# Kernel tuning notes

Hardware: AMD Instinct MI355X
Metric: run time of the kernel (lower is better)

Reference implementation:

```python
import jax, jax.numpy as jnp
import numpy as np

VOCAB_SIZE = 8192
EMBED_DIM = 256


def setup_inputs() -> dict:
    key = jax.random.key(0)
    k1, k2 = jax.random.split(key)
    N = 16384  # batch(512) * num_slots(8) * tokens_per_slot(4)
    z = jax.random.normal(k1, (N, EMBED_DIM), dtype=jnp.float32)
    codebook = jax.random.normal(k2, (VOCAB_SIZE, EMBED_DIM), dtype=jnp.float32)
    return {"z": z, "codebook": codebook}


def reference(z, codebook):
    # Squared-distance cdist via the expansion ||z||^2 + ||e||^2 - 2 z.e^T
    z_sq = jnp.sum(z * z, axis=1, keepdims=True)            # [N, 1]
    e_sq = jnp.sum(codebook * codebook, axis=1)              # [V]
    dist = z_sq + e_sq - 2.0 * jnp.matmul(z, codebook.T)     # [N, V]
    tokens = jnp.argmin(dist, axis=-1)                       # [N] int
    z_q = codebook[tokens]                                   # [N, E] gather
    # one-hot reference count (side statistic in the original forward)
    ref_count = jnp.zeros((VOCAB_SIZE,), dtype=jnp.float32).at[tokens].add(1.0)
    return tokens, z_q, ref_count
```

## Files before the change

kernel.cpp:

```cpp
#include <hip/hip_runtime.h>
#include <math.h>

#define N_ROWS 16384
#define VOCAB  8192
#define EMB    256

#define BM 128
#define BV 128
#define BK 64
#define VSPLIT 8
#define VRANGE (VOCAB / VSPLIT)
#define NVT    (VRANGE / BV)
#define TAU 0.15f

typedef _Float16 half8 __attribute__((ext_vector_type(8)));
typedef _Float16 half4 __attribute__((ext_vector_type(4)));
typedef float floatx4 __attribute__((ext_vector_type(4)));

__device__ __forceinline__ void load_lds16(const _Float16* g, _Float16* l) {
    __builtin_amdgcn_global_load_lds(
        (const __attribute__((address_space(1))) void*)g,
        (__attribute__((address_space(3))) void*)l, 16, 0, 0);
}

__global__ void prep_kernel(const float* __restrict__ z, const float* __restrict__ cb,
                            _Float16* __restrict__ zh, _Float16* __restrict__ ch,
                            float* __restrict__ esq, float* __restrict__ cnt,
                            unsigned long long* __restrict__ rkey,
                            int* __restrict__ flagcnt) {
    const int b = blockIdx.x, t = threadIdx.x;
    if (b < VOCAB / 4) {
        const int row  = b * 4 + (t >> 6);
        const int lane = t & 63;
        const float4 f = *(const float4*)(cb + (size_t)row * EMB + lane * 4);
        half4 h;
        h.x = (_Float16)f.x; h.y = (_Float16)f.y; h.z = (_Float16)f.z; h.w = (_Float16)f.w;
        *(half4*)(ch + (size_t)row * EMB + lane * 4) = h;
        float s = f.x * f.x + f.y * f.y + f.z * f.z + f.w * f.w;
        #pragma unroll
        for (int off = 32; off > 0; off >>= 1) s += __shfl_down(s, off, 64);
        if (lane == 0) esq[row] = s;
        if (t < 4) cnt[b * 4 + t] = 0.0f;
        if (t >= 8 && t < 16) rkey[b * 8 + (t - 8)] = ~0ull;
        if (b == 0 && t == 4) flagcnt[0] = 0;
        if (b == 0 && t == 5) flagcnt[1] = 0;
    } else {
        const size_t idx4 = (size_t)(b - VOCAB / 4) * 256 + t;
        const float4 f = *(const float4*)(z + idx4 * 4);
        half4 h;
        h.x = (_Float16)f.x; h.y = (_Float16)f.y; h.z = (_Float16)f.z; h.w = (_Float16)f.w;
        *(half4*)(zh + idx4 * 4) = h;
    }
}

__global__ __launch_bounds__(256, 2)
void mfma_dist_kernel(const _Float16* __restrict__ zh, const _Float16* __restrict__ ch,
                      const float* __restrict__ esq,
                      float* __restrict__ pd1, float* __restrict__ pd2,
                      float* __restrict__ pd3,
                      int* __restrict__ pi1, int* __restrict__ pi2) {
    __shared__ _Float16 zs[BM * BK];
    __shared__ _Float16 cs[BV * BK];
    float* sc_d1 = (float*)zs;
    float* sc_d2 = sc_d1 + BM * 2;
    float* sc_d3 = sc_d2 + BM * 2;
    int*   sc_i1 = (int*)(sc_d3 + BM * 2);
    int*   sc_i2 = sc_i1 + BM * 2;

    const int row0  = blockIdx.x * BM;
    const int vbase = blockIdx.y * VRANGE;

    const int tid  = threadIdx.x;
    const int w    = tid >> 6;
    const int lane = tid & 63;
    const int lr   = lane & 15;
    const int quad = lane >> 4;
    const int mh   = (w >> 1) * 64;
    const int vh   = (w & 1) * 64;

    const int q7   = quad ^ (lr & 7);
    const int offA0 = q7 * 8;
    const int offA1 = (4 ^ q7) * 8;
    int rA[4], rB[4];
    #pragma unroll
    for (int i = 0; i < 4; ++i) { rA[i] = (mh + i * 16 + lr) * BK; rB[i] = (vh + i * 16 + lr) * BK; }

    const int schunk = (lane & 7) ^ (lane >> 3);
    const _Float16* zsrc = zh + (size_t)(row0 + w * 32 + (lane >> 3)) * EMB + schunk * 8;

    float m1[16], m2[16], m3[16];
    #pragma unroll
    for (int t = 0; t < 16; ++t) { m1[t] = -INFINITY; m2[t] = -INFINITY; m3[t] = -INFINITY; }

    float ev[4];
    #pragma unroll
    for (int j = 0; j < 4; ++j) ev[j] = esq[vbase + vh + j * 16 + lr];

    for (int vt = 0; vt < NVT; ++vt) {
        const int v0 = vbase + vt * BV;
        const _Float16* csrc = ch + (size_t)(v0 + w * 32 + (lane >> 3)) * EMB + schunk * 8;

        floatx4 acc[4][4];
        #pragma unroll
        for (int j = 0; j < 4; ++j) {
            const float e2 = -0.5f * ev[j];
            #pragma unroll
            for (int i = 0; i < 4; ++i) acc[i][j] = (floatx4)e2;
        }
        float evn[4];
        {
            const int vtn = (vt + 1 < NVT) ? vt + 1 : vt;
            #pragma unroll
            for (int j = 0; j < 4; ++j) evn[j] = esq[vbase + vtn * BV + vh + j * 16 + lr];
        }

        #pragma unroll 1
        for (int kt = 0; kt < EMB / BK; ++kt) {
            const int ko = kt * BK;
            #pragma unroll
            for (int q = 0; q < 4; ++q) {
                load_lds16(zsrc + (size_t)q * 8 * EMB + ko, &zs[w * 2048 + q * 512]);
                load_lds16(csrc + (size_t)q * 8 * EMB + ko, &cs[w * 2048 + q * 512]);
            }
            __syncthreads();

            #pragma unroll
            for (int s = 0; s < 2; ++s) {
                const int off = s ? offA1 : offA0;
                half8 a[4];
                #pragma unroll
                for (int i = 0; i < 4; ++i) a[i] = *(const half8*)&zs[rA[i] + off];
                #pragma unroll
                for (int j = 0; j < 4; ++j) {
                    const half8 b = *(const half8*)&cs[rB[j] + off];
                    #pragma unroll
                    for (int i = 0; i < 4; ++i)
                        acc[i][j] = __builtin_amdgcn_mfma_f32_16x16x32_f16(a[i], b, acc[i][j], 0, 0, 0);
                }
            }
            __syncthreads();
        }

        #pragma unroll
        for (int i = 0; i < 4; ++i) {
            #pragma unroll
            for (int reg = 0; reg < 4; ++reg) {
                const int t = i * 4 + reg;
                #pragma unroll
                for (int j = 0; j < 4; ++j) {
                    const unsigned code = ((unsigned)vt << 2) | (unsigned)j;
                    const float a = __uint_as_float(
                        (__float_as_uint(acc[i][j][reg]) & ~31u) | code);
                    const float mid = fminf(m1[t], a);
                    m1[t] = fmaxf(m1[t], a);
                    const float lo  = fminf(m2[t], mid);
                    m2[t] = fmaxf(m2[t], mid);
                    m3[t] = fmaxf(m3[t], lo);
                }
            }
        }
        #pragma unroll
        for (int j = 0; j < 4; ++j) ev[j] = evn[j];
    }

    int i1[16], i2[16];
    #pragma unroll
    for (int t = 0; t < 16; ++t) {
        const unsigned c1 = __float_as_uint(m1[t]) & 31u;
        const unsigned c2 = __float_as_uint(m2[t]) & 31u;
        i1[t] = vbase + (int)(c1 >> 2) * BV + vh + (int)(c1 & 3u) * 16 + lr;
        i2[t] = vbase + (int)(c2 >> 2) * BV + vh + (int)(c2 & 3u) * 16 + lr;
    }

    #pragma unroll
    for (int t = 0; t < 16; ++t) {
        float a1 = m1[t], a2 = m2[t], a3 = m3[t]; int ii1 = i1[t], ii2 = i2[t];
        #pragma unroll
        for (int off = 1; off < 16; off <<= 1) {
            const float o1 = __shfl_xor(a1, off, 64);
            const float o2 = __shfl_xor(a2, off, 64);
            const float o3 = __shfl_xor(a3, off, 64);
            const int  oi1 = __shfl_xor(ii1, off, 64);
            const int  oi2 = __shfl_xor(ii2, off, 64);
            const bool g1 = o1 > a1, g2 = o1 > a2, g3 = o1 > a3;
            a3  = g2 ? a2  : (g3 ? o1  : a3);
            a2  = g1 ? a1  : (g2 ? o1  : a2);
            ii2 = g1 ? ii1 : (g2 ? oi1 : ii2);
            a1  = g1 ? o1  : a1;
            ii1 = g1 ? oi1 : ii1;
            const bool h2 = o2 > a2, h3 = o2 > a3;
            a3  = h2 ? a2  : (h3 ? o2 : a3);
            a2  = h2 ? o2  : a2;
            ii2 = h2 ? oi2 : ii2;
            a3 = fmaxf(a3, o3);
        }
        m1[t] = a1; m2[t] = a2; m3[t] = a3; i1[t] = ii1; i2[t] = ii2;
    }
    if (lr == 0) {
        #pragma unroll
        for (int t = 0; t < 16; ++t) {
            const int r = mh + (t >> 2) * 16 + quad * 4 + (t & 3);
            sc_d1[r * 2 + (w & 1)] = m1[t];
            sc_d2[r * 2 + (w & 1)] = m2[t];
            sc_d3[r * 2 + (w & 1)] = m3[t];
            sc_i1[r * 2 + (w & 1)] = i1[t];
            sc_i2[r * 2 + (w & 1)] = i2[t];
        }
    }
    __syncthreads();
    if (tid < BM) {
        float a1 = sc_d1[tid * 2], a2 = sc_d2[tid * 2], a3 = sc_d3[tid * 2];
        int  ii1 = sc_i1[tid * 2], ii2 = sc_i2[tid * 2];
        const float o1 = sc_d1[tid * 2 + 1], o2 = sc_d2[tid * 2 + 1], o3 = sc_d3[tid * 2 + 1];
        const int  oi1 = sc_i1[tid * 2 + 1], oi2 = sc_i2[tid * 2 + 1];
        {
            const bool g1 = o1 > a1, g2 = o1 > a2, g3 = o1 > a3;
            a3  = g2 ? a2  : (g3 ? o1  : a3);
            a2  = g1 ? a1  : (g2 ? o1  : a2);
            ii2 = g1 ? ii1 : (g2 ? oi1 : ii2);
            a1  = g1 ? o1  : a1;
            ii1 = g1 ? oi1 : ii1;
            const bool h2 = o2 > a2, h3 = o2 > a3;
            a3  = h2 ? a2  : (h3 ? o2 : a3);
            a2  = h2 ? o2  : a2;
            ii2 = h2 ? oi2 : ii2;
            a3 = fmaxf(a3, o3);
        }
        const size_t o = (size_t)blockIdx.y * N_ROWS + row0 + tid;
        pd1[o] = -2.0f * a1; pd2[o] = -2.0f * a2; pd3[o] = -2.0f * a3;
        pi1[o] = ii1; pi2[o] = ii2;
    }
}

__global__ void combine_kernel(const float* __restrict__ pd1, const float* __restrict__ pd2,
                               const float* __restrict__ pd3, const int* __restrict__ pi1,
                               const float* __restrict__ cb,
                               float* __restrict__ tokens, float* __restrict__ zq,
                               float* __restrict__ cnt,
                               int* __restrict__ flagcnt,
                               int* __restrict__ clist, int* __restrict__ flist) {
    const int wave = threadIdx.x >> 6;
    const int lane = threadIdx.x & 63;
    const int row  = blockIdx.x * 4 + wave;

    float g1 = INFINITY, g2 = INFINITY, mind3 = INFINITY; int gi = 0;
    #pragma unroll
    for (int s = 0; s < VSPLIT; ++s) {
        const size_t o = (size_t)s * N_ROWS + row;
        const float od1 = pd1[o], od2 = pd2[o], od3 = pd3[o]; const int oi1 = pi1[o];
        if (od1 < g1) { g2 = fminf(g1, od2); g1 = od1; gi = oi1; }
        else          { g2 = fminf(g2, od1); }
        mind3 = fminf(mind3, od3);
    }
    if ((g2 - g1) < TAU) {
        if (lane == 0) {
            if (mind3 >= g1 + TAU) {
                const int pos = atomicAdd(&flagcnt[0], 1);
                clist[pos] = row;
            } else {
                const int pos = atomicAdd(&flagcnt[1], 1);
                flist[pos] = row;
            }
        }
        return;
    }
    if (lane == 0) {
        tokens[row] = (float)gi;
        atomicAdd(&cnt[gi], 1.0f);
    }
    const float4 v = *(const float4*)(cb + (size_t)gi * EMB + lane * 4);
    *(float4*)(zq + (size_t)row * EMB + lane * 4) = v;
}

__global__ void rescue_cand_kernel(const int* __restrict__ flagcnt,
                                   const int* __restrict__ clist,
                                   const float* __restrict__ z, const float* __restrict__ cb,
                                   const float* __restrict__ esq,
                                   const int* __restrict__ pi1, const int* __restrict__ pi2,
                                   float* __restrict__ tokens, float* __restrict__ zq,
                                   float* __restrict__ cnt) {
    const int n    = flagcnt[0];
    const int w    = threadIdx.x >> 6;
    const int lane = threadIdx.x & 63;
    const int c    = lane >> 2;
    const int s    = lane & 3;

    for (int f = blockIdx.x * 4 + w; f < n; f += gridDim.x * 4) {
        const int row = clist[f];
        const size_t po = (size_t)(c & 7) * N_ROWS + row;
        const int cidx = (c < 8) ? pi1[po] : pi2[po];

        const float* zr = z  + (size_t)row  * EMB + s * 64;
        const float* cr = cb + (size_t)cidx * EMB + s * 64;
        float p0 = 0.0f, p1 = 0.0f, p2 = 0.0f, p3 = 0.0f;
        #pragma unroll
        for (int k = 0; k < 4; ++k) {
            const float4 z0 = *(const float4*)(zr + k * 16 + 0);
            const float4 c0 = *(const float4*)(cr + k * 16 + 0);
            const float4 z1 = *(const float4*)(zr + k * 16 + 4);
            const float4 c1 = *(const float4*)(cr + k * 16 + 4);
            const float4 z2 = *(const float4*)(zr + k * 16 + 8);
            const float4 c2 = *(const float4*)(cr + k * 16 + 8);
            const float4 z3 = *(const float4*)(zr + k * 16 + 12);
            const float4 c3 = *(const float4*)(cr + k * 16 + 12);
            p0 += z0.x * c0.x + z0.y * c0.y + z0.z * c0.z + z0.w * c0.w;
            p1 += z1.x * c1.x + z1.y * c1.y + z1.z * c1.z + z1.w * c1.w;
            p2 += z2.x * c2.x + z2.y * c2.y + z2.z * c2.z + z2.w * c2.w;
            p3 += z3.x * c3.x + z3.y * c3.y + z3.z * c3.z + z3.w * c3.w;
        }
        float p = (p0 + p1) + (p2 + p3);
        p += __shfl_xor(p, 1, 64);
        p += __shfl_xor(p, 2, 64);

        float bd = esq[cidx] - 2.0f * p;
        int   bv = cidx;
        #pragma unroll
        for (int off = 4; off < 64; off <<= 1) {
            const float od = __shfl_xor(bd, off, 64);
            const int   ov = __shfl_xor(bv, off, 64);
            if (od < bd || (od == bd && ov < bv)) { bd = od; bv = ov; }
        }
        if (lane == 0) {
            tokens[row] = (float)bv;
            atomicAdd(&cnt[bv], 1.0f);
        }
        const float4 c4 = *(const float4*)(cb + (size_t)bv * EMB + lane * 4);
        *(float4*)(zq + (size_t)row * EMB + lane * 4) = c4;
    }
}

#define RBV 64
#define RSPLIT 4
#define NTILE (VOCAB / RBV)
__global__ __launch_bounds__(256, 2)
void rescue_full_kernel(const int* __restrict__ flagcnt, const int* __restrict__ flist,
                        const float* __restrict__ z, const float* __restrict__ cb,
                        const float* __restrict__ esq,
                        unsigned long long* __restrict__ rkey) {
    const int n = __builtin_amdgcn_readfirstlane(flagcnt[1]);
    if (n == 0) return;

    __shared__ float cs[RBV][EMB];

    const int tile = blockIdx.x >> 2;
    const int rs   = blockIdx.x & 3;
    const int c0   = tile * RBV;
    const int tid  = threadIdx.x;
    const int w    = tid >> 6;
    const int lane = tid & 63;
    const int g    = lane >> 2;
    const int s    = lane & 3;

    #pragma unroll
    for (int i = 0; i < 16; ++i) {
        const int code = i * 4 + w;
        const float4 v = *(const float4*)(cb + (size_t)(c0 + code) * EMB + lane * 4);
        *(float4*)&cs[code][(lane ^ (code & 7)) * 4] = v;
    }
    __syncthreads();

    const int nq = (n + 3) >> 2;
    const int q0 = (rs << 2) | w;
    if (q0 >= nq) return;

    float ev[4];
    #pragma unroll
    for (int gs = 0; gs < 4; ++gs) ev[gs] = esq[c0 + gs * 16 + g];

    for (int q = q0; q < nq; q += 16) {
        int rows[4];
        #pragma unroll
        for (int r = 0; r < 4; ++r) {
            const int fi = q * 4 + r;
            rows[r] = __builtin_amdgcn_readfirstlane(flist[fi < n ? fi : 0]);
        }

        float p[4][4];
        #pragma unroll
        for (int gs = 0; gs < 4; ++gs)
            #pragma unroll
            for (int r = 0; r < 4; ++r) p[gs][r] = 0.0f;

        #pragma unroll
        for (int kb = 0; kb < 4; ++kb) {
            #pragma unroll
            for (int kk = 0; kk < 4; ++kk) {
                const int dbase = (kb * 4 + kk) * 16 + s * 4;
                float4 zv[4];
                #pragma unroll
                for (int r = 0; r < 4; ++r)
                    zv[r] = *(const float4*)(z + (size_t)rows[r] * EMB + dbase);
                const int dq = (kb * 4 + kk) * 4 + s;
                #pragma unroll
                for (int gs = 0; gs < 4; ++gs) {
                    const int code = gs * 16 + g;
                    const float4 c4 = *(const float4*)&cs[code][(dq ^ (code & 7)) * 4];
                    #pragma unroll
                    for (int r = 0; r < 4; ++r)
                        p[gs][r] += zv[r].x * c4.x + zv[r].y * c4.y
                                  + zv[r].z * c4.z + zv[r].w * c4.w;
                }
            }
        }

        #pragma unroll
        for (int gs = 0; gs < 4; ++gs)
            #pragma unroll
            for (int r = 0; r < 4; ++r) {
                float t = p[gs][r];
                t += __shfl_xor(t, 1, 64);
                t += __shfl_xor(t, 2, 64);
                p[gs][r] = t;
            }

        #pragma unroll
        for (int r = 0; r < 4; ++r) {
            float bd = INFINITY; int bv = 0;
            #pragma unroll
            for (int gs = 0; gs < 4; ++gs) {
                const float d = ev[gs] - 2.0f * p[gs][r];
                const int v = c0 + gs * 16 + g;
                if (d < bd) { bd = d; bv = v; }
            }
            #pragma unroll
            for (int off = 4; off < 64; off <<= 1) {
                const float od = __shfl_xor(bd, off, 64);
                const int   ov = __shfl_xor(bv, off, 64);
                if (od < bd || (od == bd && ov < bv)) { bd = od; bv = ov; }
            }
            if (lane == 0 && q * 4 + r < n) {
                unsigned int u = __float_as_uint(bd);
                u = (u & 0x80000000u) ? ~u : (u | 0x80000000u);
                atomicMin(rkey + rows[r], ((unsigned long long)u << 32) | (unsigned int)bv);
            }
        }
    }
}

__global__ void rescue_write_kernel(const int* __restrict__ flagcnt,
                                    const int* __restrict__ flist,
                                    const unsigned long long* __restrict__ rkey,
                                    const float* __restrict__ cb,
                                    float* __restrict__ tokens, float* __restrict__ zq,
                                    float* __restrict__ cnt) {
    const int w    = threadIdx.x >> 6;
    const int lane = threadIdx.x & 63;
    const int n = flagcnt[1];
    for (int f = blockIdx.x * 4 + w; f < n; f += gridDim.x * 4) {
        const int row = flist[f];
        const int v = (int)(unsigned int)(rkey[row] & 0xFFFFFFFFull);
        if (lane == 0) {
            tokens[row] = (float)v;
            atomicAdd(&cnt[v], 1.0f);
        }
        const float4 c4 = *(const float4*)(cb + (size_t)v * EMB + lane * 4);
        *(float4*)(zq + (size_t)row * EMB + lane * 4) = c4;
    }
}

__global__ void esq_kernel(const float* __restrict__ cb, float* __restrict__ esq) {
    const int wave = threadIdx.x >> 6;
    const int lane = threadIdx.x & 63;
    const int row  = blockIdx.x * 4 + wave;
    const float4 v = *(const float4*)(cb + (size_t)row * EMB + lane * 4);
    float s = v.x * v.x + v.y * v.y + v.z * v.z + v.w * v.w;
    #pragma unroll
    for (int off = 32; off > 0; off >>= 1) s += __shfl_down(s, off, 64);
    if (lane == 0) esq[row] = s;
}

#define FLSTR 36
__global__ __launch_bounds__(256, 2)
void fb_dist_kernel(const float* __restrict__ z, const float* __restrict__ cb,
                    const float* __restrict__ esq,
                    float* __restrict__ pdist, int* __restrict__ pidx) {
    __shared__ float zs[BM][FLSTR];
    __shared__ float es[BV][FLSTR];
    __shared__ float rdist[16][16];
    __shared__ int   ridx [16][16];
    const int row0 = blockIdx.x * BM, vbase = blockIdx.y * VRANGE;
    const int tid = threadIdx.x, wave = tid >> 6, lane = tid & 63;
    const int wly = (lane >> 3) & 7, wlx = lane & 7;
    const int wbase = (wave >> 1) * 64, cbase = (wave & 1) * 64;
    const int arow = wbase + wly, bcol = cbase + wlx;
    const int rowSlot = (wave >> 1) * 8 + wly, colSlot = (wave & 1) * 8 + wlx;
    const int sc4 = tid & 7, sr0 = tid >> 3;
    float best[8]; int bidx[8];
    #pragma unroll
    for (int i = 0; i < 8; ++i) { best[i] = INFINITY; bidx[i] = 0; }
    for (int vt = 0; vt < NVT; ++vt) {
        const int v0 = vbase + vt * BV;
        float acc[8][8];
        #pragma unroll
        for (int i = 0; i < 8; ++i)
            #pragma unroll
            for (int j = 0; j < 8; ++j) acc[i][j] = 0.0f;
        #pragma unroll 1
        for (int kt = 0; kt < EMB / 32; ++kt) {
            #pragma unroll
            for (int t = 0; t < 4; ++t) {
                const int r = sr0 + 32 * t;
                *(float4*)&zs[r][sc4 * 4] = *(const float4*)(z  + (size_t)(row0 + r) * EMB + kt * 32 + sc4 * 4);
                *(float4*)&es[r][sc4 * 4] = *(const float4*)(cb + (size_t)(v0 + r) * EMB + kt * 32 + sc4 * 4);
            }
            __syncthreads();
            #pragma unroll 1
            for (int k0 = 0; k0 < 8; ++k0) {
                const int kk = k0 * 4;
                float a[8][4];
                #pragma unroll
                for (int i = 0; i < 8; ++i) {
                    const float4 a4 = *(const float4*)&zs[arow + 8 * i][kk];
                    a[i][0] = a4.x; a[i][1] = a4.y; a[i][2] = a4.z; a[i][3] = a4.w;
                }
                #pragma unroll
                for (int j = 0; j < 8; ++j) {
                    const float4 b4 = *(const float4*)&es[bcol + 8 * j][kk];
                    #pragma unroll
                    for (int i = 0; i < 8; ++i) {
                        acc[i][j] += a[i][0] * b4.x; acc[i][j] += a[i][1] * b4.y;
                        acc[i][j] += a[i][2] * b4.z; acc[i][j] += a[i][3] * b4.w;
                    }
                }
            }
            __syncthreads();
        }
        #pragma unroll
        for (int j = 0; j < 8; ++j) {
            const int v = v0 + bcol + 8 * j;
            const float evv = esq[v];
            #pragma unroll
            for (int i = 0; i < 8; ++i) {
                const float d = evv - 2.0f * acc[i][j];
                if (d < best[i]) { best[i] = d; bidx[i] = v; }
            }
        }
    }
    for (int i = 0; i < 8; ++i) {
        rdist[rowSlot][colSlot] = best[i];
        ridx [rowSlot][colSlot] = bidx[i];
        __syncthreads();
        if (colSlot == 0) {
            float bd = rdist[rowSlot][0]; int bi = ridx[rowSlot][0];
            #pragma unroll
            for (int t = 1; t < 16; ++t) {
                const float d = rdist[rowSlot][t]; const int ii = ridx[rowSlot][t];
                if (d < bd || (d == bd && ii < bi)) { bd = d; bi = ii; }
            }
            const int row = row0 + wbase + 8 * i + wly;
            pdist[(size_t)blockIdx.y * N_ROWS + row] = bd;
            pidx [(size_t)blockIdx.y * N_ROWS + row] = bi;
        }
        __syncthreads();
    }
}

__global__ void fb_combine_kernel(const float* __restrict__ pdist, const int* __restrict__ pidx,
                                  const float* __restrict__ cb,
                                  float* __restrict__ tokens, float* __restrict__ zq,
                                  float* __restrict__ cnt) {
    const int wave = threadIdx.x >> 6, lane = threadIdx.x & 63;
    const int row = blockIdx.x * 4 + wave;
    float bd = INFINITY; int bi = 0;
    #pragma unroll
    for (int s = 0; s < VSPLIT; ++s) {
        const float d = pdist[(size_t)s * N_ROWS + row];
        const int ii  = pidx [(size_t)s * N_ROWS + row];
        if (d < bd || (d == bd && ii < bi)) { bd = d; bi = ii; }
    }
    if (lane == 0) { tokens[row] = (float)bi; atomicAdd(&cnt[bi], 1.0f); }
    const float4 v = *(const float4*)(cb + (size_t)bi * EMB + lane * 4);
    *(float4*)(zq + (size_t)row * EMB + lane * 4) = v;
}

extern "C" void kernel_launch(void* const* d_in, const int* in_sizes, int n_in,
                              void* d_out, int out_size, void* d_ws, size_t ws_size,
                              hipStream_t stream) {
    const float* z  = (const float*)d_in[0];
    const float* cb = (const float*)d_in[1];

    float* out    = (float*)d_out;
    float* tokens = out;
    float* zq     = out + N_ROWS;
    float* cnt    = out + N_ROWS + (size_t)N_ROWS * EMB;

    const size_t ZE = (size_t)N_ROWS * EMB, CE = (size_t)VOCAB * EMB, P = (size_t)VSPLIT * N_ROWS;
    const size_t NEED = (ZE + CE) * sizeof(_Float16) + VOCAB * 4
                      + 5 * P * 4 + (size_t)N_ROWS * 8 + 256 + 2 * (size_t)N_ROWS * 4;

    if (ws_size >= NEED) {
        char* p = (char*)d_ws;
        _Float16* zh = (_Float16*)p;            p += ZE * 2;
        _Float16* ch = (_Float16*)p;            p += CE * 2;
        float* esq   = (float*)p;               p += VOCAB * 4;
        float* pd1   = (float*)p;               p += P * 4;
        float* pd2   = (float*)p;               p += P * 4;
        float* pd3   = (float*)p;               p += P * 4;
        int*   pi1   = (int*)p;                 p += P * 4;
        int*   pi2   = (int*)p;                 p += P * 4;
        unsigned long long* rkey = (unsigned long long*)p;  p += (size_t)N_ROWS * 8;
        int*   flagcnt = (int*)p;               p += 256;
        int*   clist = (int*)p;                 p += (size_t)N_ROWS * 4;
        int*   flist = (int*)p;

        prep_kernel<<<VOCAB / 4 + (int)(ZE / 4 / 256), 256, 0, stream>>>(
            z, cb, zh, ch, esq, cnt, rkey, flagcnt);
        mfma_dist_kernel<<<dim3(N_ROWS / BM, VSPLIT), 256, 0, stream>>>(
            zh, ch, esq, pd1, pd2, pd3, pi1, pi2);
        combine_kernel<<<N_ROWS / 4, 256, 0, stream>>>(
            pd1, pd2, pd3, pi1, cb, tokens, zq, cnt, flagcnt, clist, flist);
        rescue_cand_kernel<<<512, 256, 0, stream>>>(
            flagcnt, clist, z, cb, esq, pi1, pi2, tokens, zq, cnt);
        rescue_full_kernel<<<NTILE * RSPLIT, 256, 0, stream>>>(
            flagcnt, flist, z, cb, esq, rkey);
        rescue_write_kernel<<<32, 256, 0, stream>>>(
            flagcnt, flist, rkey, cb, tokens, zq, cnt);
    } else {
        float* esq   = (float*)d_ws;
        float* pdist = esq + VOCAB;
        int*   pidx  = (int*)(pdist + P);
        hipMemsetAsync(cnt, 0, VOCAB * sizeof(float), stream);
        esq_kernel<<<VOCAB / 4, 256, 0, stream>>>(cb, esq);
        fb_dist_kernel<<<dim3(N_ROWS / BM, VSPLIT), 256, 0, stream>>>(z, cb, esq, pdist, pidx);
        fb_combine_kernel<<<N_ROWS / 4, 256, 0, stream>>>(pdist, pidx, cb, tokens, zq, cnt);
    }
}
```

Before: 209.1 us.

## Process two codebook tiles per iteration to reuse z fragments across 256 columns

```diff
diff --git a/kernel.cpp b/kernel.cpp
--- a/kernel.cpp
+++ b/kernel.cpp
@@ -60,7 +60,8 @@
                       float* __restrict__ pd3,
                       int* __restrict__ pi1, int* __restrict__ pi2) {
     __shared__ _Float16 zs[BM * BK];
-    __shared__ _Float16 cs[BV * BK];
+    __shared__ _Float16 csA[BV * BK];
+    __shared__ _Float16 csB[BV * BK];
     float* sc_d1 = (float*)zs;
     float* sc_d2 = sc_d1 + BM * 2;
     float* sc_d3 = sc_d2 + BM * 2;
@@ -92,26 +93,34 @@
     #pragma unroll
     for (int t = 0; t < 16; ++t) { m1[t] = -INFINITY; m2[t] = -INFINITY; m3[t] = -INFINITY; }
 
-    float ev[4];
-    #pragma unroll
-    for (int j = 0; j < 4; ++j) ev[j] = esq[vbase + vh + j * 16 + lr];
-
-    for (int vt = 0; vt < NVT; ++vt) {
-        const int v0 = vbase + vt * BV;
-        const _Float16* csrc = ch + (size_t)(v0 + w * 32 + (lane >> 3)) * EMB + schunk * 8;
-
-        floatx4 acc[4][4];
+    float evA[4], evB[4];
+    #pragma unroll
+    for (int j = 0; j < 4; ++j) {
+        evA[j] = esq[vbase + vh + j * 16 + lr];
+        evB[j] = esq[vbase + BV + vh + j * 16 + lr];
+    }
+
+    for (int it = 0; it < NVT / 2; ++it) {
+        const int vA = vbase + it * 2 * BV;
+        const _Float16* csrcA = ch + (size_t)(vA + w * 32 + (lane >> 3)) * EMB + schunk * 8;
+        const _Float16* csrcB = csrcA + (size_t)BV * EMB;
+
+        floatx4 accA[4][4], accB[4][4];
         #pragma unroll
         for (int j = 0; j < 4; ++j) {
-            const float e2 = -0.5f * ev[j];
-            #pragma unroll
-            for (int i = 0; i < 4; ++i) acc[i][j] = (floatx4)e2;
-        }
-        float evn[4];
+            const float eA = -0.5f * evA[j];
+            const float eB = -0.5f * evB[j];
+            #pragma unroll
+            for (int i = 0; i < 4; ++i) { accA[i][j] = (floatx4)eA; accB[i][j] = (floatx4)eB; }
+        }
+        float evnA[4], evnB[4];
         {
-            const int vtn = (vt + 1 < NVT) ? vt + 1 : vt;
-            #pragma unroll
-            for (int j = 0; j < 4; ++j) evn[j] = esq[vbase + vtn * BV + vh + j * 16 + lr];
+            const int itn = (it + 1 < NVT / 2) ? it + 1 : it;
+            #pragma unroll
+            for (int j = 0; j < 4; ++j) {
+                evnA[j] = esq[vbase + itn * 2 * BV + vh + j * 16 + lr];
+                evnB[j] = esq[vbase + itn * 2 * BV + BV + vh + j * 16 + lr];
+            }
         }
 
         #pragma unroll 1
@@ -119,8 +128,9 @@
             const int ko = kt * BK;
             #pragma unroll
             for (int q = 0; q < 4; ++q) {
-                load_lds16(zsrc + (size_t)q * 8 * EMB + ko, &zs[w * 2048 + q * 512]);
-                load_lds16(csrc + (size_t)q * 8 * EMB + ko, &cs[w * 2048 + q * 512]);
+                load_lds16(zsrc  + (size_t)q * 8 * EMB + ko, &zs [w * 2048 + q * 512]);
+                load_lds16(csrcA + (size_t)q * 8 * EMB + ko, &csA[w * 2048 + q * 512]);
+                load_lds16(csrcB + (size_t)q * 8 * EMB + ko, &csB[w * 2048 + q * 512]);
             }
             __syncthreads();
 
@@ -132,10 +142,17 @@
                 for (int i = 0; i < 4; ++i) a[i] = *(const half8*)&zs[rA[i] + off];
                 #pragma unroll
                 for (int j = 0; j < 4; ++j) {
-                    const half8 b = *(const half8*)&cs[rB[j] + off];
+                    const half8 bA = *(const half8*)&csA[rB[j] + off];
                     #pragma unroll
                     for (int i = 0; i < 4; ++i)
-                        acc[i][j] = __builtin_amdgcn_mfma_f32_16x16x32_f16(a[i], b, acc[i][j], 0, 0, 0);
+                        accA[i][j] = __builtin_amdgcn_mfma_f32_16x16x32_f16(a[i], bA, accA[i][j], 0, 0, 0);
+                }
+                #pragma unroll
+                for (int j = 0; j < 4; ++j) {
+                    const half8 bB = *(const half8*)&csB[rB[j] + off];
+                    #pragma unroll
+                    for (int i = 0; i < 4; ++i)
+                        accB[i][j] = __builtin_amdgcn_mfma_f32_16x16x32_f16(a[i], bB, accB[i][j], 0, 0, 0);
                 }
             }
             __syncthreads();
@@ -148,19 +165,30 @@
                 const int t = i * 4 + reg;
                 #pragma unroll
                 for (int j = 0; j < 4; ++j) {
-                    const unsigned code = ((unsigned)vt << 2) | (unsigned)j;
+                    const unsigned code = ((unsigned)it << 3) | (unsigned)j;
                     const float a = __uint_as_float(
-                        (__float_as_uint(acc[i][j][reg]) & ~31u) | code);
+                        (__float_as_uint(accA[i][j][reg]) & ~31u) | code);
                     const float mid = fminf(m1[t], a);
                     m1[t] = fmaxf(m1[t], a);
                     const float lo  = fminf(m2[t], mid);
                     m2[t] = fmaxf(m2[t], mid);
                     m3[t] = fmaxf(m3[t], lo);
                 }
-            }
-        }
-        #pragma unroll
-        for (int j = 0; j < 4; ++j) ev[j] = evn[j];
+                #pragma unroll
+                for (int j = 0; j < 4; ++j) {
+                    const unsigned code = ((unsigned)it << 3) | 4u | (unsigned)j;
+                    const float a = __uint_as_float(
+                        (__float_as_uint(accB[i][j][reg]) & ~31u) | code);
+                    const float mid = fminf(m1[t], a);
+                    m1[t] = fmaxf(m1[t], a);
+                    const float lo  = fminf(m2[t], mid);
+                    m2[t] = fmaxf(m2[t], mid);
+                    m3[t] = fmaxf(m3[t], lo);
+                }
+            }
+        }
+        #pragma unroll
+        for (int j = 0; j < 4; ++j) { evA[j] = evnA[j]; evB[j] = evnB[j]; }
     }
 
     int i1[16], i2[16];
```

After: 193.1 us (median of 3 runs). 7.6% less time.
